# Optimization experiments

Measured on AMD Instinct MI355X. Metric: run time of the kernel, lower is better.

## Reference

```python
import jax, jax.numpy as jnp
import numpy as np

N_NODES = 50000
N_EDGES = 800000
IN_DIM = 13
HID = 64
LAYER_DIMS = [(IN_DIM, HID), (HID, HID), (HID, HID), (HID, HID), (HID, 1)]


def setup_inputs() -> dict:
    key = jax.random.key(0)
    ks = jax.random.split(key, 20)
    x = jax.random.normal(ks[0], (N_NODES, IN_DIM), dtype=jnp.float32)
    edge_index = jax.random.randint(ks[1], (2, N_EDGES), 0, N_NODES)
    edge_weight = jax.random.uniform(ks[2], (N_EDGES,), dtype=jnp.float32)
    inp = {"x": x, "edge_index": edge_index, "edge_weight": edge_weight}
    for i, (di, do) in enumerate(LAYER_DIMS):
        s = 1.0 / np.sqrt(di)
        inp[f"Wrel{i}"] = (jax.random.normal(ks[3 + 3 * i], (di, do)) * s).astype(jnp.float32)
        inp[f"brel{i}"] = jnp.zeros((do,), dtype=jnp.float32)
        inp[f"Wroot{i}"] = (jax.random.normal(ks[4 + 3 * i], (di, do)) * s).astype(jnp.float32)
    return inp


def _graph_conv(x, src, dst, ew, Wrel, brel, Wroot):
    # PyG GraphConv: out = lin_rel(sum_{j in N(i)} w_e * x_j) + lin_root(x_i)
    msgs = ew[:, None] * x[src]                      # [E, d_in] gather
    aggr = jax.ops.segment_sum(msgs, dst, num_segments=N_NODES)  # [N, d_in]
    return aggr @ Wrel + brel + x @ Wroot


def reference(x, edge_index, edge_weight,
              Wrel0, brel0, Wroot0,
              Wrel1, brel1, Wroot1,
              Wrel2, brel2, Wroot2,
              Wrel3, brel3, Wroot3,
              Wrel4, brel4, Wroot4):
    src, dst = edge_index[0], edge_index[1]  # source_to_target flow
    params = [
        (Wrel0, brel0, Wroot0),
        (Wrel1, brel1, Wroot1),
        (Wrel2, brel2, Wroot2),
        (Wrel3, brel3, Wroot3),
        (Wrel4, brel4, Wroot4),
    ]
    h = x
    for Wr, br, Ws in params[:-1]:
        h = jax.nn.relu(_graph_conv(h, src, dst, edge_weight, Wr, br, Ws))
    Wr, br, Ws = params[-1]
    h = _graph_conv(h, src, dst, edge_weight, Wr, br, Ws)
    return jax.nn.sigmoid(h)  # [N, 1]
```

## Files before the change

kernel.cpp:

```cpp
#include <hip/hip_runtime.h>
#include <math.h>

#define N_NODES 50000
#define N_EDGES 800000
#define NBUCKET 196
#define CHUNK 4096
#define NCHUNK 196
#define SCAN_N (NBUCKET * NCHUNK)
#define SB_A 151
#define SB_B 196
#define NSB (SB_A + SB_B)
#define EPT 16
#define CAP_FINE 8192
#define MAXEPAD (N_EDGES + N_NODES * 4)
#define XELEMS (N_NODES * 13)
#define XCONV_B 32

typedef __attribute__((ext_vector_type(8))) _Float16 f16x8;
typedef __attribute__((ext_vector_type(4))) float f32x4;

__device__ __forceinline__ int roundup4(int v) { return (v + 3) & ~3; }

__device__ __forceinline__ float upw(int e) {
    unsigned short u = (unsigned short)(((unsigned)e) >> 16);
    return (float)__builtin_bit_cast(_Float16, u);
}


__device__ __forceinline__ int block_excl_scan(int v, int* wsum) {
    int t = threadIdx.x, lane = t & 63, w = t >> 6;
    int sc = v;
    #pragma unroll
    for (int o = 1; o < 64; o <<= 1) {
        int u = __shfl_up(sc, o, 64);
        if (lane >= o) sc += u;
    }
    if (lane == 63) wsum[w] = sc;
    __syncthreads();
    int add = 0;
    #pragma unroll
    for (int j = 0; j < 4; ++j) if (j < w) add += wsum[j];
    return add + sc - v;
}


__global__ void hist_kernel(const int* __restrict__ dst, int* __restrict__ h,
                            int* __restrict__ counts,
                            const float* __restrict__ W1r, const float* __restrict__ W1o,
                            const float* __restrict__ W2r, const float* __restrict__ W2o,
                            const float* __restrict__ W3r, const float* __restrict__ W3o,
                            _Float16* __restrict__ wfrag,
                            const float* __restrict__ x, _Float16* __restrict__ xh) {
    if (blockIdx.x >= NCHUNK + 3) {
        int b = blockIdx.x - (NCHUNK + 3);
        for (int i = b * 256 + threadIdx.x; i < XELEMS; i += XCONV_B * 256)
            xh[i] = (_Float16)x[i];
        return;
    }
    if (blockIdx.x >= NCHUNK) {
        int b = blockIdx.x - NCHUNK, t = threadIdx.x;
        const float* Wr = (b == 0) ? W1r : (b == 1) ? W2r : W3r;
        const float* Wo = (b == 0) ? W1o : (b == 1) ? W2o : W3o;
        _Float16* out = wfrag + (size_t)b * 8192;
        for (int i = t; i < 1024; i += 256) {
            int frag = i >> 6, lane = i & 63;
            int m = frag >> 3, ct = (frag >> 1) & 3, ks = frag & 1;
            int col = ct * 16 + (lane & 15);
            int kb = ks * 32 + (lane >> 4) * 8;
            const float* W = m ? Wo : Wr;
            f16x8 v;
            #pragma unroll
            for (int j = 0; j < 8; ++j) v[j] = (_Float16)W[(kb + j) * 64 + col];
            *(f16x8*)&out[(size_t)i * 8] = v;
        }
        return;
    }
    __shared__ int hist[NBUCKET];
    for (int i = threadIdx.x; i < NBUCKET; i += 256) hist[i] = 0;
    __syncthreads();
    int base = blockIdx.x * CHUNK;
    int n = min(CHUNK, N_EDGES - base);
    for (int k = threadIdx.x; k < n; k += 256) {
        int d = dst[base + k];
        atomicAdd(&hist[d >> 8], 1);
        atomicAdd(&counts[d], 1);
    }
    __syncthreads();
    for (int i = threadIdx.x; i < NBUCKET; i += 256)
        h[i * NCHUNK + blockIdx.x] = hist[i];
}


__global__ void scan_sums(const int* __restrict__ h, const int* __restrict__ counts,
                          int* __restrict__ blocksums) {
    __shared__ int wsum[4];
    int bid = blockIdx.x, t = threadIdx.x;
    int v;
    if (bid < SB_A) {
        int i = bid * 256 + t;
        v = (i < SCAN_N) ? h[i] : 0;
    } else {
        int j = (bid - SB_A) * 256 + t;
        v = (j < N_NODES) ? roundup4(counts[j]) : 0;
    }
    int lane = t & 63, w = t >> 6;
    int s = v;
    #pragma unroll
    for (int o = 1; o < 64; o <<= 1) s += __shfl_xor(s, o, 64);
    if (lane == 0) wsum[w] = s;
    __syncthreads();
    if (t == 0) blocksums[bid] = wsum[0] + wsum[1] + wsum[2] + wsum[3];
}

__global__ void scan_apply(int* __restrict__ h, int* __restrict__ offs,
                           const int* __restrict__ counts,
                           const int* __restrict__ blocksums) {
    __shared__ int sblk[NSB + 1];
    __shared__ int wsum[4];
    int bid = blockIdx.x, t = threadIdx.x;
    if (t < 64) {
        int carry = 0;
        for (int c = 0; c < NSB; c += 64) {
            int i = c + t;
            int v = (i < NSB) ? blocksums[i] : 0;
            int sc = v;
            #pragma unroll
            for (int o = 1; o < 64; o <<= 1) {
                int u = __shfl_up(sc, o, 64);
                if (t >= o) sc += u;
            }
            if (i < NSB) sblk[i] = carry + sc - v;
            carry += __shfl(sc, 63, 64);
        }
        if (t == 0) sblk[NSB] = carry;
    }
    __syncthreads();
    int v;
    if (bid < SB_A) {
        int i = bid * 256 + t;
        v = (i < SCAN_N) ? h[i] : 0;
        int e = block_excl_scan(v, wsum);
        int base = sblk[bid];
        if (i < SCAN_N) h[i] = e + base;
    } else {
        int j = (bid - SB_A) * 256 + t;
        v = (j < N_NODES) ? roundup4(counts[j]) : 0;
        int e = block_excl_scan(v, wsum);
        int base = sblk[bid] - sblk[SB_A];
        if (j < N_NODES) {
            offs[j] = e + base;
            if (j == N_NODES - 1) offs[N_NODES] = e + base + v;
        }
    }
}


__launch_bounds__(256, 4)
__global__ void scatter_coarse(const int* __restrict__ src, const int* __restrict__ dst,
                               const float* __restrict__ ew, const int* __restrict__ hs,
                               int2* __restrict__ ecoarse) {
    __shared__ int cnt[NBUCKET];
    __shared__ int excl[NBUCKET];
    __shared__ int cur[NBUCKET];
    __shared__ int gbase[NBUCKET];
    __shared__ int wsum[4];
    __shared__ int2 stage[CHUNK];

    int t = threadIdx.x;
    int base = blockIdx.x * CHUNK;
    int n = min(CHUNK, N_EDGES - base);

    for (int i = t; i < NBUCKET; i += 256) {
        cnt[i] = 0;
        gbase[i] = hs[i * NCHUNK + blockIdx.x];
    }
    __syncthreads();

    int rx[EPT];
    float rw[EPT];
    #pragma unroll
    for (int j = 0; j < EPT; ++j) {
        int k = t + j * 256;
        if (k < n) {
            int e = base + k;
            int d = dst[e];
            rx[j] = (d << 16) | src[e];
            rw[j] = ew[e];
            atomicAdd(&cnt[d >> 8], 1);
        }
    }
    __syncthreads();

    {
        int v = (t < NBUCKET) ? cnt[t] : 0;
        int e = block_excl_scan(v, wsum);
        if (t < NBUCKET) { excl[t] = e; cur[t] = e; }
    }
    __syncthreads();

    #pragma unroll
    for (int j = 0; j < EPT; ++j) {
        int k = t + j * 256;
        if (k < n) {
            int b = ((unsigned)rx[j]) >> 24;
            int p = atomicAdd(&cur[b], 1);
            stage[p] = make_int2(rx[j], __float_as_int(rw[j]));
        }
    }
    __syncthreads();

    for (int k = t; k < n; k += 256) {
        int2 r = stage[k];
        int b = ((unsigned)r.x) >> 24;
        ecoarse[gbase[b] + (k - excl[b])] = r;
    }
}


__launch_bounds__(256)
__global__ void fine_sort(const int* __restrict__ h, const int* __restrict__ offs,
                          const int2* __restrict__ ecoarse, int* __restrict__ epack) {
    int b = blockIdx.x, t = threadIdx.x;
    __shared__ int cur[256];
    __shared__ int stage[CAP_FINE];
    int bstartU = h[b * NCHUNK];
    int bendU = (b == NBUCKET - 1) ? N_EDGES : h[(b + 1) * NCHUNK];
    int nbU = bendU - bstartU;
    int P = offs[b << 8];
    int nodeEnd = min((b + 1) << 8, N_NODES);
    int plen = offs[nodeEnd] - P;
    int dstv = (b << 8) + t;
    cur[t] = (dstv < N_NODES) ? offs[dstv] - P : 0;
    __syncthreads();
    if (plen <= CAP_FINE) {
        for (int k = t; k < plen; k += 256) stage[k] = 0;
        __syncthreads();
        for (int k = t; k < nbU; k += 256) {
            int2 r = ecoarse[bstartU + k];
            int d = (((unsigned)r.x) >> 16) & 255;
            unsigned short hw = __builtin_bit_cast(unsigned short, (_Float16)__int_as_float(r.y));
            int p = atomicAdd(&cur[d], 1);
            stage[p] = (r.x & 0xFFFF) | ((int)hw << 16);
        }
        __syncthreads();
        for (int k = t; k < plen; k += 256) epack[P + k] = stage[k];
    } else {
        for (int k = t; k < plen; k += 256) epack[P + k] = 0;
        __syncthreads();
        for (int k = t; k < nbU; k += 256) {
            int2 r = ecoarse[bstartU + k];
            int d = (((unsigned)r.x) >> 16) & 255;
            unsigned short hw = __builtin_bit_cast(unsigned short, (_Float16)__int_as_float(r.y));
            int p = atomicAdd(&cur[d], 1);
            epack[P + p] = (r.x & 0xFFFF) | ((int)hw << 16);
        }
    }
}


__device__ __forceinline__ float bcast(float v, int k) {
    return __int_as_float(__builtin_amdgcn_readlane(__float_as_int(v), k));
}


__launch_bounds__(256)
__global__ void layer0_fused(const int* __restrict__ offs, const int* __restrict__ epack,
                             const _Float16* __restrict__ xh, const float* __restrict__ Wrel,
                             const float* __restrict__ bias, const float* __restrict__ Wroot,
                             _Float16* __restrict__ h0) {
    int wid = (blockIdx.x * blockDim.x + threadIdx.x) >> 6;
    int lane = threadIdx.x & 63;
    float wr[13], wo[13];
    #pragma unroll
    for (int k = 0; k < 13; ++k) {
        wr[k] = Wrel[k * 64 + lane];
        wo[k] = Wroot[k * 64 + lane];
    }
    float bc = bias[lane];
    int q = lane >> 4, f = lane & 15;
    int beg = offs[wid], end = offs[wid + 1];
    float acc = 0.f;
    bool fv = (f < 13);
    int i = beg + q;
    for (; i + 4 < end; i += 8) {
        int e0 = epack[i], e1 = epack[i + 4];
        float v0 = fv ? (float)xh[(size_t)(e0 & 0xFFFF) * 13 + f] : 0.f;
        float v1 = fv ? (float)xh[(size_t)(e1 & 0xFFFF) * 13 + f] : 0.f;
        acc = fmaf(upw(e0), v0, acc);
        acc = fmaf(upw(e1), v1, acc);
    }
    if (i < end) {
        int e = epack[i];
        float v = fv ? (float)xh[(size_t)(e & 0xFFFF) * 13 + f] : 0.f;
        acc = fmaf(upw(e), v, acc);
    }
    acc += __shfl_xor(acc, 16, 64);
    acc += __shfl_xor(acc, 32, 64);
    float hv = (lane < 13) ? (float)xh[(size_t)wid * 13 + lane] : 0.f;
    float a0 = bc, a1 = 0.f, a2 = 0.f, a3 = 0.f;
    #pragma unroll
    for (int k = 0; k + 2 <= 13; k += 2) {
        a0 = fmaf(bcast(acc, k), wr[k], a0);
        a1 = fmaf(bcast(hv, k), wo[k], a1);
        a2 = fmaf(bcast(acc, k + 1), wr[k + 1], a2);
        a3 = fmaf(bcast(hv, k + 1), wo[k + 1], a3);
    }
    a0 = fmaf(bcast(acc, 12), wr[12], a0);
    a1 = fmaf(bcast(hv, 12), wo[12], a1);
    float o = fmaxf((a0 + a2) + (a1 + a3), 0.f);
    h0[(size_t)wid * 64 + lane] = (_Float16)o;
}


template <bool FINAL>
__launch_bounds__(256)
__global__ void layer_fused(const int* __restrict__ offs, const int* __restrict__ epack,
                            const _Float16* __restrict__ hin, const _Float16* __restrict__ wfrag_l,
                            const float* __restrict__ bias, _Float16* __restrict__ hout,
                            const float* __restrict__ Wrel4, const float* __restrict__ Wroot4,
                            float* __restrict__ z, float* __restrict__ root) {
    __shared__ __align__(16) _Float16 aggrHi[32][72];
    __shared__ __align__(16) _Float16 aggrLo[32][72];
    __shared__ float zpart[4][32], rpart[4][32];
    int t = threadIdx.x;
    int rowbase = blockIdx.x * 32;
    int w = t >> 6, lane = t & 63;

    f16x8 br0 = *(const f16x8*)&wfrag_l[(size_t)(((0 * 4 + w) * 2 + 0) * 64 + lane) * 8];
    f16x8 br1 = *(const f16x8*)&wfrag_l[(size_t)(((0 * 4 + w) * 2 + 1) * 64 + lane) * 8];
    f16x8 bo0 = *(const f16x8*)&wfrag_l[(size_t)(((1 * 4 + w) * 2 + 0) * 64 + lane) * 8];
    f16x8 bo1 = *(const f16x8*)&wfrag_l[(size_t)(((1 * 4 + w) * 2 + 1) * 64 + lane) * 8];
    int r = lane & 15, kq = lane >> 4;
    float bc = bias[w * 16 + r];
    float w4rv = 0.f, w4ov = 0.f;
    if (FINAL) { w4rv = Wrel4[w * 16 + r]; w4ov = Wroot4[w * 16 + r]; }

    int qw = t >> 4, l = t & 15;
    int hi8 = l >> 3, f8 = l & 7;
    #pragma unroll
    for (int rr = 0; rr < 2; ++rr) {
        int node = rowbase + qw + rr * 16;
        float a[8] = {0.f, 0.f, 0.f, 0.f, 0.f, 0.f, 0.f, 0.f};
        if (node < N_NODES) {
            int beg = offs[node], end = offs[node + 1];
            int i = beg;
            for (; i + 4 < end; i += 8) {
                int4 pk0 = *(const int4*)(epack + i);
                int4 pk1 = *(const int4*)(epack + i + 4);
                int e0 = hi8 ? pk0.z : pk0.x;
                int e1 = hi8 ? pk0.w : pk0.y;
                int e2 = hi8 ? pk1.z : pk1.x;
                int e3 = hi8 ? pk1.w : pk1.y;
                f16x8 r0 = *(const f16x8*)(hin + (size_t)(e0 & 0xFFFF) * 64 + f8 * 8);
                f16x8 r1 = *(const f16x8*)(hin + (size_t)(e1 & 0xFFFF) * 64 + f8 * 8);
                f16x8 r2 = *(const f16x8*)(hin + (size_t)(e2 & 0xFFFF) * 64 + f8 * 8);
                f16x8 r3 = *(const f16x8*)(hin + (size_t)(e3 & 0xFFFF) * 64 + f8 * 8);
                float w0 = upw(e0), w1 = upw(e1), w2 = upw(e2), w3 = upw(e3);
                #pragma unroll
                for (int j = 0; j < 8; ++j) {
                    a[j] = fmaf(w0, (float)r0[j], a[j]);
                    a[j] = fmaf(w1, (float)r1[j], a[j]);
                    a[j] = fmaf(w2, (float)r2[j], a[j]);
                    a[j] = fmaf(w3, (float)r3[j], a[j]);
                }
            }
            if (i < end) {
                int4 pk = *(const int4*)(epack + i);
                int e0 = hi8 ? pk.z : pk.x;
                int e1 = hi8 ? pk.w : pk.y;
                f16x8 r0 = *(const f16x8*)(hin + (size_t)(e0 & 0xFFFF) * 64 + f8 * 8);
                f16x8 r1 = *(const f16x8*)(hin + (size_t)(e1 & 0xFFFF) * 64 + f8 * 8);
                float w0 = upw(e0), w1 = upw(e1);
                #pragma unroll
                for (int j = 0; j < 8; ++j) {
                    a[j] = fmaf(w0, (float)r0[j], a[j]);
                    a[j] = fmaf(w1, (float)r1[j], a[j]);
                }
            }
        }
        #pragma unroll
        for (int j = 0; j < 8; ++j) a[j] += __shfl_xor(a[j], 8, 64);
        f16x8 wv;
        #pragma unroll
        for (int j = 0; j < 8; ++j) {
            _Float16 hh = (_Float16)a[j];
            wv[j] = hi8 ? (_Float16)(a[j] - (float)hh) : hh;
        }
        int row = qw + rr * 16;
        _Float16* dstp = hi8 ? &aggrLo[row][f8 * 8] : &aggrHi[row][f8 * 8];
        *(f16x8*)dstp = wv;
    }
    __syncthreads();

    #pragma unroll
    for (int g = 0; g < 2; ++g) {
        int lr = g * 16 + r;
        int grow = min(rowbase + lr, N_NODES - 1);
        f32x4 acc = {bc, bc, bc, bc};
        {
            f16x8 Ah = *(const f16x8*)&aggrHi[lr][0 * 32 + kq * 8];
            f16x8 Al = *(const f16x8*)&aggrLo[lr][0 * 32 + kq * 8];
            f16x8 Ar = *(const f16x8*)&hin[(size_t)grow * 64 + 0 * 32 + kq * 8];
            acc = __builtin_amdgcn_mfma_f32_16x16x32_f16(Ah, br0, acc, 0, 0, 0);
            acc = __builtin_amdgcn_mfma_f32_16x16x32_f16(Al, br0, acc, 0, 0, 0);
            acc = __builtin_amdgcn_mfma_f32_16x16x32_f16(Ar, bo0, acc, 0, 0, 0);
        }
        {
            f16x8 Ah = *(const f16x8*)&aggrHi[lr][1 * 32 + kq * 8];
            f16x8 Al = *(const f16x8*)&aggrLo[lr][1 * 32 + kq * 8];
            f16x8 Ar = *(const f16x8*)&hin[(size_t)grow * 64 + 1 * 32 + kq * 8];
            acc = __builtin_amdgcn_mfma_f32_16x16x32_f16(Ah, br1, acc, 0, 0, 0);
            acc = __builtin_amdgcn_mfma_f32_16x16x32_f16(Al, br1, acc, 0, 0, 0);
            acc = __builtin_amdgcn_mfma_f32_16x16x32_f16(Ar, bo1, acc, 0, 0, 0);
        }
        if (FINAL) {
            #pragma unroll
            for (int j = 0; j < 4; ++j) {
                float o = fmaxf(acc[j], 0.f);
                float zz = o * w4rv, rv = o * w4ov;
                #pragma unroll
                for (int m = 1; m < 16; m <<= 1) {
                    zz += __shfl_xor(zz, m, 64);
                    rv += __shfl_xor(rv, m, 64);
                }
                if (r == 0) {
                    int lrow = g * 16 + (lane >> 4) * 4 + j;
                    zpart[w][lrow] = zz;
                    rpart[w][lrow] = rv;
                }
            }
        } else {
            #pragma unroll
            for (int j = 0; j < 4; ++j) {
                int row = rowbase + g * 16 + (lane >> 4) * 4 + j;
                if (row < N_NODES)
                    hout[(size_t)row * 64 + w * 16 + r] = (_Float16)fmaxf(acc[j], 0.f);
            }
        }
    }
    if (FINAL) {
        __syncthreads();
        if (t < 32) {
            int row = rowbase + t;
            if (row < N_NODES) {
                z[row] = zpart[0][t] + zpart[1][t] + zpart[2][t] + zpart[3][t];
                root[row] = rpart[0][t] + rpart[1][t] + rpart[2][t] + rpart[3][t];
            }
        }
    }
}


__launch_bounds__(256)
__global__ void final_aggr(const int* __restrict__ offs, const int* __restrict__ epack,
                           const float* __restrict__ z, const float* __restrict__ root,
                           const float* __restrict__ b4, float* __restrict__ out) {
    int tid = blockIdx.x * blockDim.x + threadIdx.x;
    int node = tid >> 2, g = tid & 3;
    if (node >= N_NODES) return;
    int beg = offs[node], end = offs[node + 1];
    float a = 0.f;
    int i = beg + g;
    for (; i + 4 < end; i += 8) {
        int e0 = epack[i], e1 = epack[i + 4];
        a = fmaf(upw(e0), z[e0 & 0xFFFF], a);
        a = fmaf(upw(e1), z[e1 & 0xFFFF], a);
    }
    if (i < end) {
        int e = epack[i];
        a = fmaf(upw(e), z[e & 0xFFFF], a);
    }
    a += __shfl_xor(a, 1, 64);
    a += __shfl_xor(a, 2, 64);
    if (g == 0) {
        float v = a + b4[0] + root[node];
        out[node] = 1.f / (1.f + expf(-v));
    }
}


extern "C" void kernel_launch(void* const* d_in, const int* in_sizes, int n_in,
                              void* d_out, int out_size, void* d_ws, size_t ws_size,
                              hipStream_t stream) {
    const float* x = (const float*)d_in[0];
    const int* eidx = (const int*)d_in[1];
    const float* ew = (const float*)d_in[2];
    const float* Wrel[5];
    const float* brel[5];
    const float* Wroot[5];
    for (int i = 0; i < 5; ++i) {
        Wrel[i] = (const float*)d_in[3 + 3 * i];
        brel[i] = (const float*)d_in[4 + 3 * i];
        Wroot[i] = (const float*)d_in[5 + 3 * i];
    }
    const int* src = eidx;
    const int* dst = eidx + N_EDGES;
    float* out = (float*)d_out;

    char* ws = (char*)d_ws;
    size_t off = 0;
    auto alloc = [&](size_t bytes) -> void* {
        void* p = ws + off;
        off = (off + bytes + 255) & ~(size_t)255;
        return p;
    };
    int* h = (int*)alloc((size_t)(SCAN_N + 256) * 4);
    int* blocksums = (int*)alloc(512 * 4);
    int* counts = (int*)alloc((size_t)N_NODES * 4);
    int* offs = (int*)alloc((size_t)(N_NODES + 1) * 4);
    int* epack = (int*)alloc((size_t)MAXEPAD * 4);
    _Float16* h0 = (_Float16*)alloc((size_t)N_NODES * 64 * 2);
    _Float16* h1 = (_Float16*)alloc((size_t)N_NODES * 64 * 2);
    _Float16* wfrag = (_Float16*)alloc((size_t)3 * 8192 * 2);
    _Float16* xh = (_Float16*)alloc((size_t)XELEMS * 2);
    float* z = (float*)alloc((size_t)N_NODES * 4);
    float* root = (float*)alloc((size_t)N_NODES * 4);
    int2* ecoarse = (int2*)h0;
    (void)ws_size; (void)in_sizes; (void)n_in; (void)out_size;

    hipMemsetAsync(counts, 0, (size_t)N_NODES * 4, stream);
    hist_kernel<<<NCHUNK + 3 + XCONV_B, 256, 0, stream>>>(dst, h, counts,
                                                Wrel[1], Wroot[1], Wrel[2], Wroot[2],
                                                Wrel[3], Wroot[3], wfrag, x, xh);
    scan_sums<<<NSB, 256, 0, stream>>>(h, counts, blocksums);
    scan_apply<<<NSB, 256, 0, stream>>>(h, offs, counts, blocksums);
    scatter_coarse<<<NCHUNK, 256, 0, stream>>>(src, dst, ew, h, ecoarse);
    fine_sort<<<NBUCKET, 256, 0, stream>>>(h, offs, ecoarse, epack);

    const int NODE_BLOCKS = N_NODES * 64 / 256;
    const int FB = (N_NODES + 31) / 32;

    layer0_fused<<<NODE_BLOCKS, 256, 0, stream>>>(offs, epack, xh, Wrel[0], brel[0], Wroot[0], h0);

    layer_fused<false><<<FB, 256, 0, stream>>>(offs, epack, h0, wfrag, brel[1], h1,
                                               nullptr, nullptr, nullptr, nullptr);
    layer_fused<false><<<FB, 256, 0, stream>>>(offs, epack, h1, wfrag + 8192, brel[2], h0,
                                               nullptr, nullptr, nullptr, nullptr);
    layer_fused<true><<<FB, 256, 0, stream>>>(offs, epack, h0, wfrag + 16384, brel[3], nullptr,
                                              Wrel[4], Wroot[4], z, root);

    final_aggr<<<(N_NODES * 4 + 255) / 256, 256, 0, stream>>>(offs, epack, z, root, brel[4], out);
}
```

Baseline: 174.4 us.

## Fuse two-pass scan into single-pass decoupled scan with status flags

Replaces the separate block-sum and apply scan kernels with one kernel where each block publishes its aggregate through a flagged status word, and later blocks spin-wait on predecessor flags to build their base offset. This removes one kernel launch and a global round trip of block sums. The status array is zeroed by the existing memset. The design relies on earlier blocks being scheduled before later ones to avoid deadlock, and on 347 blocks fitting on the device at once.

New measurement: 184.7 us. 1.06x slower.

```diff
diff --git a/kernel.cpp b/kernel.cpp
--- a/kernel.cpp
+++ b/kernel.cpp
@@ -91,9 +91,10 @@
 }
 
 
-__global__ void scan_sums(const int* __restrict__ h, const int* __restrict__ counts,
-                          int* __restrict__ blocksums) {
+__global__ void scan_fused(int* __restrict__ h, int* __restrict__ offs,
+                           const int* __restrict__ counts, int* __restrict__ status) {
     __shared__ int wsum[4];
+    __shared__ int blkagg, sbase;
     int bid = blockIdx.x, t = threadIdx.x;
     int v;
     if (bid < SB_A) {
@@ -103,50 +104,33 @@
         int j = (bid - SB_A) * 256 + t;
         v = (j < N_NODES) ? roundup4(counts[j]) : 0;
     }
-    int lane = t & 63, w = t >> 6;
-    int s = v;
-    #pragma unroll
-    for (int o = 1; o < 64; o <<= 1) s += __shfl_xor(s, o, 64);
-    if (lane == 0) wsum[w] = s;
-    __syncthreads();
-    if (t == 0) blocksums[bid] = wsum[0] + wsum[1] + wsum[2] + wsum[3];
-}
-
-__global__ void scan_apply(int* __restrict__ h, int* __restrict__ offs,
-                           const int* __restrict__ counts,
-                           const int* __restrict__ blocksums) {
-    __shared__ int sblk[NSB + 1];
-    __shared__ int wsum[4];
-    int bid = blockIdx.x, t = threadIdx.x;
+    int e = block_excl_scan(v, wsum);
+    if (t == 255) blkagg = e + v;
+    __syncthreads();
+    if (t == 0)
+        __hip_atomic_store(&status[bid], (blkagg << 1) | 1, __ATOMIC_RELEASE,
+                           __HIP_MEMORY_SCOPE_AGENT);
+    int lo = (bid < SB_A) ? 0 : SB_A;
     if (t < 64) {
-        int carry = 0;
-        for (int c = 0; c < NSB; c += 64) {
-            int i = c + t;
-            int v = (i < NSB) ? blocksums[i] : 0;
-            int sc = v;
-            #pragma unroll
-            for (int o = 1; o < 64; o <<= 1) {
-                int u = __shfl_up(sc, o, 64);
-                if (t >= o) sc += u;
-            }
-            if (i < NSB) sblk[i] = carry + sc - v;
-            carry += __shfl(sc, 63, 64);
-        }
-        if (t == 0) sblk[NSB] = carry;
-    }
-    __syncthreads();
-    int v;
+        int acc = 0;
+        for (int p = lo + t; p < bid; p += 64) {
+            int s;
+            do {
+                s = __hip_atomic_load(&status[p], __ATOMIC_ACQUIRE, __HIP_MEMORY_SCOPE_AGENT);
+            } while (!(s & 1));
+            acc += s >> 1;
+        }
+        #pragma unroll
+        for (int o = 1; o < 64; o <<= 1) acc += __shfl_xor(acc, o, 64);
+        if (t == 0) sbase = acc;
+    }
+    __syncthreads();
+    int base = sbase;
     if (bid < SB_A) {
         int i = bid * 256 + t;
-        v = (i < SCAN_N) ? h[i] : 0;
-        int e = block_excl_scan(v, wsum);
-        int base = sblk[bid];
         if (i < SCAN_N) h[i] = e + base;
     } else {
         int j = (bid - SB_A) * 256 + t;
-        v = (j < N_NODES) ? roundup4(counts[j]) : 0;
-        int e = block_excl_scan(v, wsum);
-        int base = sblk[bid] - sblk[SB_A];
         if (j < N_NODES) {
             offs[j] = e + base;
             if (j == N_NODES - 1) offs[N_NODES] = e + base + v;
@@ -505,8 +489,8 @@
         return p;
     };
     int* h = (int*)alloc((size_t)(SCAN_N + 256) * 4);
-    int* blocksums = (int*)alloc(512 * 4);
-    int* counts = (int*)alloc((size_t)N_NODES * 4);
+    int* counts = (int*)alloc((size_t)(N_NODES + NSB + 64) * 4);
+    int* status = counts + N_NODES;
     int* offs = (int*)alloc((size_t)(N_NODES + 1) * 4);
     int* epack = (int*)alloc((size_t)MAXEPAD * 4);
     _Float16* h0 = (_Float16*)alloc((size_t)N_NODES * 64 * 2);
@@ -518,12 +502,11 @@
     int2* ecoarse = (int2*)h0;
     (void)ws_size; (void)in_sizes; (void)n_in; (void)out_size;
 
-    hipMemsetAsync(counts, 0, (size_t)N_NODES * 4, stream);
+    hipMemsetAsync(counts, 0, (size_t)(N_NODES + NSB + 64) * 4, stream);
     hist_kernel<<<NCHUNK + 3 + XCONV_B, 256, 0, stream>>>(dst, h, counts,
                                                 Wrel[1], Wroot[1], Wrel[2], Wroot[2],
                                                 Wrel[3], Wroot[3], wfrag, x, xh);
-    scan_sums<<<NSB, 256, 0, stream>>>(h, counts, blocksums);
-    scan_apply<<<NSB, 256, 0, stream>>>(h, offs, counts, blocksums);
+    scan_fused<<<NSB, 256, 0, stream>>>(h, offs, counts, status);
     scatter_coarse<<<NCHUNK, 256, 0, stream>>>(src, dst, ew, h, ecoarse);
     fine_sort<<<NBUCKET, 256, 0, stream>>>(h, offs, ecoarse, epack);
 
```
